# Performance work log

Hardware: AMD Instinct MI355X
Metric: run time of the kernel (lower is better)

The kernel has to match this reference:

```python
import jax, jax.numpy as jnp
import numpy as np

N, E, D, H = 50000, 800000, 128, 8
DH = D // H  # 16
EPS_LN = 1e-5


def layer_norm(x, gamma, beta):
    mu = jnp.mean(x, axis=-1, keepdims=True)
    var = jnp.var(x, axis=-1, keepdims=True)
    return (x - mu) * jax.lax.rsqrt(var + EPS_LN) * gamma + beta


def setup_inputs() -> dict:
    key = jax.random.key(0)
    ks = jax.random.split(key, 12)
    s = 1.0 / np.sqrt(D)
    x = jax.random.normal(ks[0], (N, D), dtype=jnp.float32)
    src = jax.random.randint(ks[1], (E,), 0, N, dtype=jnp.int32)
    dst = jax.random.randint(ks[2], (E,), 0, N, dtype=jnp.int32)
    Wq = jax.random.normal(ks[3], (D, D), dtype=jnp.float32) * s
    Wk = jax.random.normal(ks[4], (D, D), dtype=jnp.float32) * s
    Wv = jax.random.normal(ks[5], (D, D), dtype=jnp.float32) * s
    Wo = jax.random.normal(ks[6], (D, D), dtype=jnp.float32) * s
    bq = jnp.zeros((D,), jnp.float32)
    bk = jnp.zeros((D,), jnp.float32)
    bv = jnp.zeros((D,), jnp.float32)
    bo = jnp.zeros((D,), jnp.float32)
    gamma1 = jnp.ones((D,), jnp.float32)
    beta1 = jnp.zeros((D,), jnp.float32)
    gamma2 = jnp.ones((D,), jnp.float32)
    beta2 = jnp.zeros((D,), jnp.float32)
    return dict(x=x, src=src, dst=dst, Wq=Wq, bq=bq, Wk=Wk, bk=bk, Wv=Wv, bv=bv,
                Wo=Wo, bo=bo, gamma1=gamma1, beta1=beta1, gamma2=gamma2, beta2=beta2)


def reference(x, src, dst, Wq, bq, Wk, bk, Wv, bv, Wo, bo, gamma1, beta1, gamma2, beta2):
    n = x.shape[0]
    Q = (x @ Wq + bq).reshape(n, H, DH)   # [N,H,Dh]
    K = (x @ Wk + bk).reshape(n, H, DH)
    V = (x @ Wv + bv).reshape(n, H, DH)
    # edge-wise QK dot: score[e,h] = sum_d K[src[e],h,d] * Q[dst[e],h,d]
    score = jnp.sum(K[src] * Q[dst], axis=-1) / np.sqrt(DH)  # [E,H]
    score = jnp.exp(jnp.clip(score, -5.0, 5.0))
    # scatter-sum weighted values and normalizer over destination nodes
    wV = jax.ops.segment_sum(V[src] * score[..., None], dst, num_segments=n)  # [N,H,Dh]
    z = jax.ops.segment_sum(score, dst, num_segments=n)                        # [N,H]
    attn = (wV / (z[..., None] + 1e-3)).reshape(n, D)
    h = layer_norm(x + attn, gamma1, beta1)
    # sublayer: h + relu(O(LN(h)))  (dropout = 0)
    h = h + jax.nn.relu(layer_norm(h, gamma2, beta2) @ Wo + bo)
    return h
```

## Files before the change

kernel.cpp:

```cpp
#include <hip/hip_runtime.h>

typedef unsigned short ushort_t;
typedef __attribute__((ext_vector_type(8))) short short8;
typedef __attribute__((ext_vector_type(4))) float floatx4;
typedef __attribute__((ext_vector_type(2))) _Float16 half2v;
typedef __attribute__((ext_vector_type(8))) _Float16 half8;

#define QSCALE 0.36067376022224085f
#define SCLIP  7.2134752044448170f

__device__ __forceinline__ unsigned h2u(half2v h) {
    union { half2v h; unsigned u; } x; x.h = h; return x.u;
}
__device__ __forceinline__ half2v u2h(unsigned u) {
    union { unsigned u; half2v h; } x; x.u = u; return x.h;
}
__device__ __forceinline__ ushort_t h2us(_Float16 h) {
    union { _Float16 h; ushort_t u; } x; x.h = h; return x.u;
}
__device__ __forceinline__ unsigned pkrtz(float a, float b) {
    auto h = __builtin_amdgcn_cvt_pkrtz(a, b);
    union { decltype(h) h2; unsigned u; } x; x.h2 = h; return x.u;
}
__device__ __forceinline__ float dot2h(half2v a, half2v b, float c) {
#if __has_builtin(__builtin_amdgcn_fdot2)
    return __builtin_amdgcn_fdot2(a, b, c, false);
#else
    return c + (float)a[0] * (float)b[0] + (float)a[1] * (float)b[1];
#endif
}
__device__ __forceinline__ half2v pk_shfl_add(half2v a, int m) {
    unsigned o = (unsigned)__shfl_xor((int)h2u(a), m, 64);
    return a + u2h(o);
}

__global__ __launch_bounds__(256) void transpose_swz(
    const float* __restrict__ Wq, const float* __restrict__ Wk,
    const float* __restrict__ Wv, const float* __restrict__ Wo,
    ushort_t* __restrict__ out, int* __restrict__ deg, int* __restrict__ gcount, int N)
{
    int flat = (blockIdx.y * gridDim.x + blockIdx.x) * 256 + threadIdx.x;
    if (flat == 0) *gcount = 0;
    for (int i = flat; i < N; i += 8192) deg[i] = 0;

    const float* W = (blockIdx.y == 0) ? Wq : (blockIdx.y == 1) ? Wk :
                     (blockIdx.y == 2) ? Wv : Wo;
    ushort_t* T = out + (size_t)blockIdx.y * 128 * 128;
    int t = blockIdx.x * 256 + threadIdx.x;
    int kg = t >> 7;
    int n  = t & 127;
    int k0 = kg * 8;
    float w[8];
    #pragma unroll
    for (int j = 0; j < 8; j++)
        w[j] = W[(size_t)(k0 + j) * 128 + n];
    int4 o;
    o.x = (int)pkrtz(w[0], w[1]);
    o.y = (int)pkrtz(w[2], w[3]);
    o.z = (int)pkrtz(w[4], w[5]);
    o.w = (int)pkrtz(w[6], w[7]);
    int sn = n >> 4, l15 = n & 15, kb = kg >> 2, quad = kg & 3;
    size_t f = ((size_t)((sn * 4 + kb) * 4 + quad)) * 128 + (size_t)l15 * 8;
    *(int4*)(T + f) = o;
}

__global__ __launch_bounds__(256) void gemm_qkv(
    const float* __restrict__ X, const ushort_t* __restrict__ Wsw,
    const float* __restrict__ bq, const float* __restrict__ bk, const float* __restrict__ bv,
    ushort_t* __restrict__ Q, ushort_t* __restrict__ KV, int M,
    const int* __restrict__ dst, int* __restrict__ deg, int E)
{
    __shared__ ushort_t Xs[64 * 136];
    int tid = threadIdx.x;
    int rowBase = blockIdx.x * 64;
    int wsel = blockIdx.y;
    const ushort_t* Wmat = Wsw + (size_t)wsel * 128 * 128;
    const float* bias = (wsel == 0) ? bq : (wsel == 1) ? bk : bv;

    {
        int nblk = gridDim.x * gridDim.y;
        int fb = blockIdx.y * gridDim.x + blockIdx.x;
        int per = (E + nblk - 1) / nblk;
        int end = min(per * (fb + 1), E);
        for (int i = per * fb + tid; i < end; i += 256)
            atomicAdd(&deg[dst[i]], 1);
    }

    int r = tid >> 4;
    int c = (tid & 15) * 8;
    for (int rr = 0; rr < 64; rr += 16) {
        int row = rowBase + rr + r;
        int rc = (row < M) ? row : (M - 1);
        const float* p = X + (size_t)rc * 128 + c;
        float4 f0 = *(const float4*)p;
        float4 f1 = *(const float4*)(p + 4);
        int4 pv;
        pv.x = (int)pkrtz(f0.x, f0.y);
        pv.y = (int)pkrtz(f0.z, f0.w);
        pv.z = (int)pkrtz(f1.x, f1.y);
        pv.w = (int)pkrtz(f1.z, f1.w);
        *(int4*)&Xs[(rr + r) * 136 + c] = pv;
    }
    __syncthreads();

    int lane = tid & 63, wave = tid >> 6;
    int wm = wave * 16;
    int l15 = lane & 15, quad = lane >> 4;
    floatx4 acc[8] = {};
    for (int kb = 0; kb < 4; kb++) {
        half8 a = *(const half8*)&Xs[(wm + l15) * 136 + kb * 32 + quad * 8];
        for (int sn = 0; sn < 8; sn++) {
            half8 b = *(const half8*)(Wmat + (size_t)(sn * 4 + kb) * 512 + lane * 8);
            acc[sn] = __builtin_amdgcn_mfma_f32_16x16x32_f16(a, b, acc[sn], 0, 0, 0);
        }
    }

    float scl = (wsel == 0) ? QSCALE : 1.0f;
    for (int sn = 0; sn < 8; sn++) {
        int col = sn * 16 + l15;
        float bia = bias[col];
        for (int rr2 = 0; rr2 < 4; rr2++) {
            int rl = wm + quad * 4 + rr2;
            Xs[rl * 136 + col] = h2us((_Float16)((acc[sn][rr2] + bia) * scl));
        }
    }
    for (int it = 0; it < 4; it++) {
        int idx = it * 64 + lane;
        int rl = idx >> 4;
        int seg = idx & 15;
        int row = rowBase + wm + rl;
        if (row < M) {
            short8 v = *(const short8*)&Xs[(wm + rl) * 136 + seg * 8];
            if (wsel == 0) {
                *(short8*)(Q + (size_t)row * 128 + seg * 8) = v;
            } else {
                *(short8*)(KV + (size_t)row * 256 + seg * 16 + ((wsel == 2) ? 8 : 0)) = v;
            }
        }
    }
}

__global__ __launch_bounds__(256) void k_alloc(const int* __restrict__ deg,
                                               int* __restrict__ offs, int* __restrict__ cursor,
                                               int* __restrict__ gcount, int n) {
    __shared__ int s[256];
    __shared__ int base;
    int tid = threadIdx.x;
    int i = blockIdx.x * 256 + tid;
    int v = (i < n) ? deg[i] : 0;
    s[tid] = v;
    __syncthreads();
    for (int d = 1; d < 256; d <<= 1) {
        int t = (tid >= d) ? s[tid - d] : 0;
        __syncthreads();
        s[tid] += t;
        __syncthreads();
    }
    int incl = s[tid];
    if (tid == 255) base = atomicAdd(gcount, incl);
    __syncthreads();
    if (i < n) {
        int o = base + incl - v;
        offs[i] = o;
        cursor[i] = o;
    }
}

__global__ __launch_bounds__(256) void k_scatter(const int* __restrict__ src, const int* __restrict__ dst,
                                                 int* __restrict__ cursor, int* __restrict__ eadj, int E) {
    int i = blockIdx.x * 256 + threadIdx.x;
    if (i < E) {
        int p = atomicAdd(&cursor[dst[i]], 1);
        eadj[p] = src[i];
    }
}

__global__ __launch_bounds__(256) void edge_attn(
    const ushort_t* __restrict__ Qb, const ushort_t* __restrict__ KV,
    const float* __restrict__ xin,
    const int* __restrict__ offs, const int* __restrict__ cur,
    const int* __restrict__ eadj,
    const float* __restrict__ g1, const float* __restrict__ be1,
    const float* __restrict__ g2, const float* __restrict__ be2,
    ushort_t* __restrict__ h1out, ushort_t* __restrict__ ln2out, int N)
{
    int wave = threadIdx.x >> 6, lane = threadIdx.x & 63;
    int n = blockIdx.x * 4 + wave;
    if (n >= N) return;
    int l15 = lane & 15, grp = lane >> 4;
    int col = l15 * 8 + grp * 2;

    uint4 qp = *(const uint4*)(Qb + (size_t)n * 128 + l15 * 8);
    half2v q0 = u2h(qp.x), q1 = u2h(qp.y), q2 = u2h(qp.z), q3 = u2h(qp.w);

    int s0 = offs[n], s1 = cur[n];

    float2 xv  = *(const float2*)(xin + (size_t)n * 128 + col);
    float2 gv  = *(const float2*)(g1 + col);
    float2 bvv = *(const float2*)(be1 + col);
    float2 g2v = *(const float2*)(g2 + col);
    float2 b2v = *(const float2*)(be2 + col);

    half2v a01 = u2h(0u), a23 = u2h(0u), a45 = u2h(0u), a67 = u2h(0u);
    float z = 0.f;
    for (int base = s0; base < s1; base += 64) {
        int cnt = min(s1 - base, 64);
        int ee = (base + lane < s1) ? eadj[base + lane] : 0;

        auto comp = [&](uint4 kk, uint4 vv, int jj) {
            float d = dot2h(u2h(kk.x), q0,
                      dot2h(u2h(kk.y), q1,
                      dot2h(u2h(kk.z), q2,
                      dot2h(u2h(kk.w), q3, 0.f))));
            d += __shfl_xor(d, 1, 64);
            float sc = fminf(SCLIP, fmaxf(-SCLIP, d));
            float e = (jj < cnt) ? exp2f(sc) : 0.f;
            _Float16 eh = (_Float16)e;
            half2v ep; ep[0] = eh; ep[1] = eh;
            a01 += u2h(vv.x) * ep;
            a23 += u2h(vv.y) * ep;
            a45 += u2h(vv.z) * ep;
            a67 += u2h(vv.w) * ep;
            z += e;
        };

        for (int j0 = 0; j0 < cnt; j0 += 16) {
            int t0 = j0 + grp;
            int sn0 = __shfl(ee, t0, 64);
            int sn1 = __shfl(ee, t0 + 4, 64);
            int sn2 = __shfl(ee, t0 + 8, 64);
            int sn3 = __shfl(ee, t0 + 12, 64);
            const ushort_t* p0 = KV + (size_t)sn0 * 256 + l15 * 16;
            const ushort_t* p1 = KV + (size_t)sn1 * 256 + l15 * 16;
            const ushort_t* p2 = KV + (size_t)sn2 * 256 + l15 * 16;
            const ushort_t* p3 = KV + (size_t)sn3 * 256 + l15 * 16;
            uint4 kk0 = *(const uint4*)p0, vv0 = *(const uint4*)(p0 + 8);
            uint4 kk1 = *(const uint4*)p1, vv1 = *(const uint4*)(p1 + 8);
            uint4 kk2 = *(const uint4*)p2, vv2 = *(const uint4*)(p2 + 8);
            uint4 kk3 = *(const uint4*)p3, vv3 = *(const uint4*)(p3 + 8);
            comp(kk0, vv0, t0);
            comp(kk1, vv1, t0 + 4);
            comp(kk2, vv2, t0 + 8);
            comp(kk3, vv3, t0 + 12);
        }
    }
    a01 = pk_shfl_add(a01, 16); a01 = pk_shfl_add(a01, 32);
    a23 = pk_shfl_add(a23, 16); a23 = pk_shfl_add(a23, 32);
    a45 = pk_shfl_add(a45, 16); a45 = pk_shfl_add(a45, 32);
    a67 = pk_shfl_add(a67, 16); a67 = pk_shfl_add(a67, 32);
    z += __shfl_xor(z, 16, 64); z += __shfl_xor(z, 32, 64);
    float inv = 1.f / (z + 1e-3f);

    half2v ap = (grp == 0) ? a01 : (grp == 1) ? a23 : (grp == 2) ? a45 : a67;
    float a0 = (float)ap[0], a1 = (float)ap[1];

    float t0 = fmaf(a0, inv, xv.x);
    float t1 = fmaf(a1, inv, xv.y);

    float s = t0 + t1, s2 = t0 * t0 + t1 * t1;
    #pragma unroll
    for (int m = 1; m < 64; m <<= 1) { s += __shfl_xor(s, m, 64); s2 += __shfl_xor(s2, m, 64); }
    float mu = s * (1.f / 128.f);
    float var = s2 * (1.f / 128.f) - mu * mu;
    float rstd = rsqrtf(var + 1e-5f);

    float h0 = (t0 - mu) * rstd * gv.x + bvv.x;
    float h1 = (t1 - mu) * rstd * gv.y + bvv.y;
    *(unsigned*)(h1out + (size_t)n * 128 + col) = pkrtz(h0, h1);

    s = h0 + h1; s2 = h0 * h0 + h1 * h1;
    #pragma unroll
    for (int m = 1; m < 64; m <<= 1) { s += __shfl_xor(s, m, 64); s2 += __shfl_xor(s2, m, 64); }
    float mu2 = s * (1.f / 128.f);
    float var2 = s2 * (1.f / 128.f) - mu2 * mu2;
    float rstd2 = rsqrtf(var2 + 1e-5f);

    float l0 = (h0 - mu2) * rstd2 * g2v.x + b2v.x;
    float l1 = (h1 - mu2) * rstd2 * g2v.y + b2v.y;
    *(unsigned*)(ln2out + (size_t)n * 128 + col) = pkrtz(l0, l1);
}

__global__ __launch_bounds__(256) void gemm_o(
    const ushort_t* __restrict__ X, const ushort_t* __restrict__ Wsw,
    const float* __restrict__ bo, const ushort_t* __restrict__ h1in,
    float* __restrict__ Out, int M)
{
    __shared__ ushort_t As[64 * 136];
    int tid = threadIdx.x;
    int rowBase = blockIdx.x * 64;
    int snBase = blockIdx.y * 4;
    int colBase = snBase * 16;

    int r = tid >> 4;
    int c = (tid & 15) * 8;
    for (int rr = 0; rr < 64; rr += 16) {
        int row = rowBase + rr + r;
        int rc = (row < M) ? row : (M - 1);
        short8 v = *(const short8*)(X + (size_t)rc * 128 + c);
        *(short8*)&As[(rr + r) * 136 + c] = v;
    }
    __syncthreads();

    int lane = tid & 63, wave = tid >> 6;
    int wm = wave * 16;
    int l15 = lane & 15, quad = lane >> 4;
    floatx4 acc[4] = {};
    for (int kb = 0; kb < 4; kb++) {
        half8 a = *(const half8*)&As[(wm + l15) * 136 + kb * 32 + quad * 8];
        for (int s = 0; s < 4; s++) {
            half8 b = *(const half8*)(Wsw + (size_t)((snBase + s) * 4 + kb) * 512 + lane * 8);
            acc[s] = __builtin_amdgcn_mfma_f32_16x16x32_f16(a, b, acc[s], 0, 0, 0);
        }
    }

    float* Cs = (float*)As;
    for (int s = 0; s < 4; s++) {
        int cl = s * 16 + l15;
        float bia = bo[colBase + cl];
        for (int rr2 = 0; rr2 < 4; rr2++) {
            int rl = wm + quad * 4 + rr2;
            Cs[rl * 68 + cl] = fmaxf(acc[s][rr2] + bia, 0.f);
        }
    }
    for (int it = 0; it < 4; it++) {
        int idx = it * 64 + lane;
        int rl = idx >> 4;
        int c4 = (idx & 15) * 4;
        int row = rowBase + wm + rl;
        if (row < M) {
            float4 v = *(const float4*)&Cs[(wm + rl) * 68 + c4];
            uint2 hp = *(const uint2*)(h1in + (size_t)row * 128 + colBase + c4);
            half2v ha = u2h(hp.x), hb = u2h(hp.y);
            v.x += (float)ha[0];
            v.y += (float)ha[1];
            v.z += (float)hb[0];
            v.w += (float)hb[1];
            *(float4*)(Out + (size_t)row * 128 + colBase + c4) = v;
        }
    }
}

extern "C" void kernel_launch(void* const* d_in, const int* in_sizes, int n_in,
                              void* d_out, int out_size, void* d_ws, size_t ws_size,
                              hipStream_t stream) {
    const int D = 128;
    const int N = in_sizes[0] / D;
    const int E = in_sizes[1];

    const float* x   = (const float*)d_in[0];
    const int*   src = (const int*)d_in[1];
    const int*   dst = (const int*)d_in[2];
    const float* Wq  = (const float*)d_in[3];
    const float* bq  = (const float*)d_in[4];
    const float* Wk  = (const float*)d_in[5];
    const float* bk  = (const float*)d_in[6];
    const float* Wv  = (const float*)d_in[7];
    const float* bv  = (const float*)d_in[8];
    const float* Wo  = (const float*)d_in[9];
    const float* bo  = (const float*)d_in[10];
    const float* g1  = (const float*)d_in[11];
    const float* be1 = (const float*)d_in[12];
    const float* g2  = (const float*)d_in[13];
    const float* be2 = (const float*)d_in[14];

    char* ws = (char*)d_ws;
    size_t o = 0;
    auto alloc = [&](size_t b) { o = (o + 255) & ~(size_t)255; size_t r = o; o += b; return r; };
    ushort_t* Qb   = (ushort_t*)(ws + alloc((size_t)N * D * 2));
    ushort_t* KVb  = (ushort_t*)(ws + alloc((size_t)N * D * 4));
    ushort_t* ln2  = (ushort_t*)(ws + alloc((size_t)N * D * 2));
    ushort_t* h1   = (ushort_t*)(ws + alloc((size_t)N * D * 2));
    ushort_t* Wt   = (ushort_t*)(ws + alloc((size_t)4 * 128 * 128 * 2));
    int*      deg  = (int*)(ws + alloc((size_t)N * 4));
    int*      offs = (int*)(ws + alloc((size_t)(N + 1) * 4));
    int*      cur  = (int*)(ws + alloc((size_t)N * 4));
    int*      gcnt = (int*)(ws + alloc((size_t)256 * 4));
    int*      eadj = (int*)(ws + alloc((size_t)E * 4));

    int nScanBlocks = (N + 255) / 256;
    int nEdgeBlocks = (E + 255) / 256;
    int nRowTiles = (N + 63) / 64;

    transpose_swz<<<dim3(8, 4), 256, 0, stream>>>(Wq, Wk, Wv, Wo, Wt, deg, gcnt, N);
    gemm_qkv<<<dim3(nRowTiles, 3), 256, 0, stream>>>(x, Wt, bq, bk, bv, Qb, KVb, N, dst, deg, E);
    k_alloc<<<nScanBlocks, 256, 0, stream>>>(deg, offs, cur, gcnt, N);
    k_scatter<<<nEdgeBlocks, 256, 0, stream>>>(src, dst, cur, eadj, E);
    edge_attn<<<(N + 3) / 4, 256, 0, stream>>>(Qb, KVb, x, offs, cur, eadj, g1, be1, g2, be2, h1, ln2, N);
    gemm_o<<<dim3(nRowTiles, 2), 256, 0, stream>>>(ln2, Wt + 3 * 128 * 128, bo, h1, (float*)d_out, N);
}
```

Baseline: 270.7 us.

## Fuse QKV projections per row tile and batch two edges per scatter thread

gemm_qkv now uses one 512-thread block per 32-row tile that computes Q, K and V together. Before, each of three blocks per tile reloaded and converted the same fp32 X rows. Results are staged in a wider shared buffer and written out to the Q and KV layouts. k_scatter now handles two edges per thread with int2 loads to cut thread count and index-load overhead. The launch bound of (512, 8) may constrain registers, and the shared-memory footprint per block grows.

```diff
diff --git a/kernel.cpp b/kernel.cpp
--- a/kernel.cpp
+++ b/kernel.cpp
@@ -64,32 +64,30 @@
     *(int4*)(T + f) = o;
 }
 
-__global__ __launch_bounds__(256) void gemm_qkv(
+__global__ __launch_bounds__(512, 8) void gemm_qkv(
     const float* __restrict__ X, const ushort_t* __restrict__ Wsw,
     const float* __restrict__ bq, const float* __restrict__ bk, const float* __restrict__ bv,
     ushort_t* __restrict__ Q, ushort_t* __restrict__ KV, int M,
     const int* __restrict__ dst, int* __restrict__ deg, int E)
 {
-    __shared__ ushort_t Xs[64 * 136];
+    __shared__ ushort_t Xs[32 * 136];
+    __shared__ ushort_t Cs[32 * 392];
     int tid = threadIdx.x;
-    int rowBase = blockIdx.x * 64;
-    int wsel = blockIdx.y;
-    const ushort_t* Wmat = Wsw + (size_t)wsel * 128 * 128;
-    const float* bias = (wsel == 0) ? bq : (wsel == 1) ? bk : bv;
+    int rowBase = blockIdx.x * 32;
 
     {
-        int nblk = gridDim.x * gridDim.y;
-        int fb = blockIdx.y * gridDim.x + blockIdx.x;
+        int nblk = gridDim.x;
+        int fb = blockIdx.x;
         int per = (E + nblk - 1) / nblk;
         int end = min(per * (fb + 1), E);
-        for (int i = per * fb + tid; i < end; i += 256)
+        for (int i = per * fb + tid; i < end; i += 512)
             atomicAdd(&deg[dst[i]], 1);
     }
 
-    int r = tid >> 4;
-    int c = (tid & 15) * 8;
-    for (int rr = 0; rr < 64; rr += 16) {
-        int row = rowBase + rr + r;
+    {
+        int r = tid >> 4;
+        int c = (tid & 15) * 8;
+        int row = rowBase + r;
         int rc = (row < M) ? row : (M - 1);
         const float* p = X + (size_t)rc * 128 + c;
         float4 f0 = *(const float4*)p;
@@ -99,43 +97,58 @@
         pv.y = (int)pkrtz(f0.z, f0.w);
         pv.z = (int)pkrtz(f1.x, f1.y);
         pv.w = (int)pkrtz(f1.z, f1.w);
-        *(int4*)&Xs[(rr + r) * 136 + c] = pv;
+        *(int4*)&Xs[r * 136 + c] = pv;
     }
     __syncthreads();
 
     int lane = tid & 63, wave = tid >> 6;
-    int wm = wave * 16;
+    int rowT = wave & 1;
+    int mg   = wave >> 1;
     int l15 = lane & 15, quad = lane >> 4;
-    floatx4 acc[8] = {};
+    floatx4 acc[6] = {};
     for (int kb = 0; kb < 4; kb++) {
-        half8 a = *(const half8*)&Xs[(wm + l15) * 136 + kb * 32 + quad * 8];
-        for (int sn = 0; sn < 8; sn++) {
-            half8 b = *(const half8*)(Wmat + (size_t)(sn * 4 + kb) * 512 + lane * 8);
-            acc[sn] = __builtin_amdgcn_mfma_f32_16x16x32_f16(a, b, acc[sn], 0, 0, 0);
-        }
-    }
-
-    float scl = (wsel == 0) ? QSCALE : 1.0f;
-    for (int sn = 0; sn < 8; sn++) {
-        int col = sn * 16 + l15;
-        float bia = bias[col];
-        for (int rr2 = 0; rr2 < 4; rr2++) {
-            int rl = wm + quad * 4 + rr2;
-            Xs[rl * 136 + col] = h2us((_Float16)((acc[sn][rr2] + bia) * scl));
-        }
-    }
-    for (int it = 0; it < 4; it++) {
-        int idx = it * 64 + lane;
-        int rl = idx >> 4;
-        int seg = idx & 15;
-        int row = rowBase + wm + rl;
+        half8 a = *(const half8*)&Xs[(rowT * 16 + l15) * 136 + kb * 32 + quad * 8];
+        #pragma unroll
+        for (int s = 0; s < 6; s++) {
+            int ct = mg * 6 + s;
+            int mat = ct >> 3;
+            int mc  = ct & 7;
+            const ushort_t* Wmat = Wsw + (size_t)mat * 128 * 128;
+            half8 b = *(const half8*)(Wmat + (size_t)(mc * 4 + kb) * 512 + lane * 8);
+            acc[s] = __builtin_amdgcn_mfma_f32_16x16x32_f16(a, b, acc[s], 0, 0, 0);
+        }
+    }
+
+    #pragma unroll
+    for (int s = 0; s < 6; s++) {
+        int ct = mg * 6 + s;
+        int mat = ct >> 3;
+        int col = ct * 16 + l15;
+        int matcol = (ct & 7) * 16 + l15;
+        const float* bias = (mat == 0) ? bq : (mat == 1) ? bk : bv;
+        float bia = bias[matcol];
+        float scl = (mat == 0) ? QSCALE : 1.0f;
+        for (int rr = 0; rr < 4; rr++) {
+            int rl = rowT * 16 + quad * 4 + rr;
+            Cs[rl * 392 + col] = h2us((_Float16)((acc[s][rr] + bia) * scl));
+        }
+    }
+    __syncthreads();
+
+    for (int it = 0; it < 3; it++) {
+        int idx = it * 512 + tid;
+        int rl = idx / 48;
+        int sg = idx - rl * 48;
+        int row = rowBase + rl;
         if (row < M) {
-            short8 v = *(const short8*)&Xs[(wm + rl) * 136 + seg * 8];
-            if (wsel == 0) {
-                *(short8*)(Q + (size_t)row * 128 + seg * 8) = v;
-            } else {
-                *(short8*)(KV + (size_t)row * 256 + seg * 16 + ((wsel == 2) ? 8 : 0)) = v;
-            }
+            short8 v = *(const short8*)&Cs[rl * 392 + sg * 8];
+            int gcol = sg * 8;
+            int mat = gcol >> 7;
+            int mc  = gcol & 127;
+            if (mat == 0)
+                *(short8*)(Q + (size_t)row * 128 + mc) = v;
+            else
+                *(short8*)(KV + (size_t)row * 256 + (mc >> 3) * 16 + ((mat == 2) ? 8 : 0)) = v;
         }
     }
 }
@@ -168,10 +181,14 @@
 
 __global__ __launch_bounds__(256) void k_scatter(const int* __restrict__ src, const int* __restrict__ dst,
                                                  int* __restrict__ cursor, int* __restrict__ eadj, int E) {
-    int i = blockIdx.x * 256 + threadIdx.x;
-    if (i < E) {
-        int p = atomicAdd(&cursor[dst[i]], 1);
-        eadj[p] = src[i];
+    int i = (blockIdx.x * 256 + threadIdx.x) * 2;
+    if (i + 1 < E) {
+        int2 s2 = *(const int2*)&src[i];
+        int2 d2 = *(const int2*)&dst[i];
+        int p0 = atomicAdd(&cursor[d2.x], 1); eadj[p0] = s2.x;
+        int p1 = atomicAdd(&cursor[d2.y], 1); eadj[p1] = s2.y;
+    } else if (i < E) {
+        int p = atomicAdd(&cursor[dst[i]], 1); eadj[p] = src[i];
     }
 }
 
@@ -378,11 +395,12 @@
     int*      eadj = (int*)(ws + alloc((size_t)E * 4));
 
     int nScanBlocks = (N + 255) / 256;
-    int nEdgeBlocks = (E + 255) / 256;
+    int nEdgeBlocks = (E / 2 + 255) / 256;
+    int nRowTiles32 = (N + 31) / 32;
     int nRowTiles = (N + 63) / 64;
 
     transpose_swz<<<dim3(8, 4), 256, 0, stream>>>(Wq, Wk, Wv, Wo, Wt, deg, gcnt, N);
-    gemm_qkv<<<dim3(nRowTiles, 3), 256, 0, stream>>>(x, Wt, bq, bk, bv, Qb, KVb, N, dst, deg, E);
+    gemm_qkv<<<nRowTiles32, 512, 0, stream>>>(x, Wt, bq, bk, bv, Qb, KVb, N, dst, deg, E);
     k_alloc<<<nScanBlocks, 256, 0, stream>>>(deg, offs, cur, gcnt, N);
     k_scatter<<<nEdgeBlocks, 256, 0, stream>>>(src, dst, cur, eadj, E);
     edge_attn<<<(N + 3) / 4, 256, 0, stream>>>(Qb, KVb, x, offs, cur, eadj, g1, be1, g2, be2, h1, ln2, N);
```

After: 270.0 us. No clear change (-0.3%).
